# Performance work log

Measured on AMD Instinct MI355X. Metric: run time of the kernel, lower is better.

Reference implementation:

```python
import jax, jax.numpy as jnp
import numpy as np

# MoE config (matches init_kwargs): dim=512, num_experts=16, top_k=2, ffn mult=4
DIM = 512
NUM_EXPERTS = 16
TOP_K = 2
HIDDEN = 4 * DIM  # FeedForward inner dim
TOKENS = 2048
LN_EPS = 1e-5


def setup_inputs() -> dict:
    key = jax.random.key(0)
    ks = jax.random.split(key, 4)
    scaled = lambda k, shape, fan_in: (
        jax.random.normal(k, shape, dtype=jnp.float32) / np.sqrt(fan_in)
    )
    return {
        "x": jax.random.normal(ks[0], (TOKENS, DIM), dtype=jnp.float32),
        # gate: Linear(dim, num_experts, bias=False)
        "Wg": scaled(ks[1], (DIM, NUM_EXPERTS), DIM),
        # per-expert FFN params stacked on leading expert axis
        "W1": scaled(ks[2], (NUM_EXPERTS, DIM, HIDDEN), DIM),
        "b1": jnp.zeros((NUM_EXPERTS, HIDDEN), jnp.float32),
        "ln_g": jnp.ones((NUM_EXPERTS, HIDDEN), jnp.float32),
        "ln_b": jnp.zeros((NUM_EXPERTS, HIDDEN), jnp.float32),
        "W2": scaled(ks[3], (NUM_EXPERTS, HIDDEN, DIM), HIDDEN),
        "b2": jnp.zeros((NUM_EXPERTS, DIM), jnp.float32),
    }


def reference(x, Wg, W1, b1, ln_g, ln_b, W2, b2):
    # ---- routing ----
    gate_logits = x @ Wg                                   # [T, E]
    w, sel = jax.lax.top_k(gate_logits, TOP_K)             # [T, k]
    # softmax over the selected-experts axis, computed in fp32 (matches dtype=torch.float)
    w = jax.nn.softmax(w.astype(jnp.float32), axis=-1).astype(x.dtype)
    n_exp = Wg.shape[1]
    # combine[t, e] = sum_k w[t, k] * 1[sel[t, k] == e]
    combine = jnp.sum(
        w[..., None] * jax.nn.one_hot(sel, n_exp, dtype=x.dtype), axis=1
    )                                                      # [T, E]

    # ---- all experts (dense, jit-friendly dispatch) ----
    # FeedForward: Linear -> SiLU -> LayerNorm -> (Dropout=identity at eval) -> Linear
    h = jnp.einsum("td,edh->eth", x, W1) + b1[:, None, :]  # [E, T, H]
    h = jax.nn.silu(h)
    mu = jnp.mean(h, axis=-1, keepdims=True)
    var = jnp.mean(jnp.square(h - mu), axis=-1, keepdims=True)
    h = (h - mu) * jax.lax.rsqrt(var + LN_EPS)
    h = h * ln_g[:, None, :] + ln_b[:, None, :]
    y = jnp.einsum("eth,ehd->etd", h, W2) + b2[:, None, :]  # [E, T, D]

    # ---- weighted combine (scatter-add equivalent) ----
    return jnp.einsum("etd,te->td", y, combine)             # [T, D]
```

## Files before the change

### kernel.cpp

```cpp
#include <hip/hip_runtime.h>
#include <hip/hip_bf16.h>

#define TOKENS 2048
#define DIM 512
#define NEXP 16
#define HID 2048
#define CAP 320
#define NTPE (CAP / 64)
#define MTILES (NEXP * NTPE)
#define NROWS (NEXP * CAP)

typedef unsigned short ushort_t;
typedef __attribute__((ext_vector_type(8))) __bf16 bf16x8;
typedef __attribute__((ext_vector_type(4))) float f32x4;

#define OFF_CNT 0
#define OFF_LTOK 1024
#define OFF_LW 21504
#define OFF_S1 41984
#define OFF_S2 62464
#define OFF_XBF 82944
#define OFF_H 2180096
#define OFF_W1T 23151616
#define OFF_W2T 56706048

__device__ __forceinline__ ushort_t f2b(float f) {
  __bf16 b = (__bf16)f;
  return __builtin_bit_cast(unsigned short, b);
}
__device__ __forceinline__ float b2f(ushort_t u) {
  return __builtin_bit_cast(float, (unsigned)u << 16);
}

__global__ __launch_bounds__(256) void wconv_k(
    const float* __restrict__ W1, const float* __restrict__ W2,
    ushort_t* __restrict__ W1t, ushort_t* __restrict__ W2t,
    int* __restrict__ counts) {
  if (blockIdx.x == 0 && blockIdx.y == 0 && threadIdx.x < NEXP)
    counts[threadIdx.x] = 0;
  int bx = blockIdx.x;
  const float* src;
  ushort_t* dst;
  int K, N;
  if (bx < 256) { src = W1; dst = W1t; K = DIM; N = HID; }
  else { src = W2; dst = W2t; K = HID; N = DIM; bx -= 256; }
  int nnb = N >> 6;
  int bn = bx % nnb, bk = bx / nnb;
  int e = blockIdx.y;
  int t = threadIdx.x;
  int w = t >> 6, l = t & 63;
  int n = bn * 64 + l;
  int k_base = bk * 64;
  int kt0 = k_base >> 5;
  int kk = w * 8;

  const float* sp = src + ((size_t)e * K + k_base + kk) * N + n;
  float v[16];
#pragma unroll
  for (int j = 0; j < 8; j++) v[j] = sp[(size_t)j * N];
#pragma unroll
  for (int j = 0; j < 8; j++) v[8 + j] = sp[(size_t)(32 + j) * N];

  size_t tb = ((size_t)(e * (N >> 4) + (n >> 4)) * (K >> 5) + kt0) * 512 +
              (n & 15) * 32 + kk;
  union { ushort_t u[8]; uint4 q; } s0, s1;
#pragma unroll
  for (int j = 0; j < 8; j++) { s0.u[j] = f2b(v[j]); s1.u[j] = f2b(v[8 + j]); }
  *(uint4*)(dst + tb) = s0.q;
  *(uint4*)(dst + tb + 512) = s1.q;
}

__global__ __launch_bounds__(256) void router_k(
    const float* __restrict__ x, const float* __restrict__ Wg,
    ushort_t* __restrict__ xbf, int* __restrict__ counts,
    int* __restrict__ ltok, float* __restrict__ lw,
    float* __restrict__ s1, float* __restrict__ s2, float* __restrict__ out) {
  int t = threadIdx.x;
  {
    float4 z = {0.f, 0.f, 0.f, 0.f};
    float4* o4 = (float4*)out + blockIdx.x * 4096 + t;
#pragma unroll
    for (int i = 0; i < 16; i++) o4[i * 256] = z;
  }
  {
    int idx = blockIdx.x * 256 + t;
    if (idx < NROWS) { s1[idx] = 0.f; s2[idx] = 0.f; }
  }

  __shared__ float xs[4][512];
  __shared__ float lg[4][16];
  __shared__ int lcnt[NEXP];
  __shared__ int ltoks[NEXP][64];
  __shared__ float lws[NEXP][64];
  __shared__ int base_s[NEXP];

  if (t < NEXP) lcnt[t] = 0;
  __syncthreads();

  int lane = t & 63, w = t >> 6;
  int dq = lane >> 2, e4 = lane & 3;
  const float* wgp = Wg + dq * NEXP + e4 * 4;

  for (int it = 0; it < 8; it++) {
    int tok = blockIdx.x * 32 + w * 8 + it;
    const float* xr = x + (size_t)tok * DIM + lane * 8;
    float4 xa = *(const float4*)xr;
    float4 xb = *(const float4*)(xr + 4);
    union { ushort_t u[8]; uint4 v; } pk;
    pk.u[0] = f2b(xa.x); pk.u[1] = f2b(xa.y); pk.u[2] = f2b(xa.z); pk.u[3] = f2b(xa.w);
    pk.u[4] = f2b(xb.x); pk.u[5] = f2b(xb.y); pk.u[6] = f2b(xb.z); pk.u[7] = f2b(xb.w);
    *(uint4*)(xbf + (size_t)tok * DIM + lane * 8) = pk.v;
    *(float4*)&xs[w][lane * 8] = xa;
    *(float4*)&xs[w][lane * 8 + 4] = xb;

    float4 a = {0.f, 0.f, 0.f, 0.f};
#pragma unroll
    for (int kk = 0; kk < 32; kk++) {
      float xv = xs[w][kk * 16 + dq];
      float4 g = *(const float4*)(wgp + kk * 16 * NEXP);
      a.x += xv * g.x; a.y += xv * g.y; a.z += xv * g.z; a.w += xv * g.w;
    }
#pragma unroll
    for (int off = 32; off >= 4; off >>= 1) {
      a.x += __shfl_down(a.x, off);
      a.y += __shfl_down(a.y, off);
      a.z += __shfl_down(a.z, off);
      a.w += __shfl_down(a.w, off);
    }
    if (lane < 4) *(float4*)&lg[w][lane * 4] = a;
    if (lane == 0) {
      int i0 = 0;
      float v0 = lg[w][0];
#pragma unroll
      for (int e = 1; e < NEXP; e++)
        if (lg[w][e] > v0) { v0 = lg[w][e]; i0 = e; }
      int i1 = -1;
      float v1 = -3.4e38f;
#pragma unroll
      for (int e = 0; e < NEXP; e++)
        if (e != i0 && lg[w][e] > v1) { v1 = lg[w][e]; i1 = e; }
      float ex = __expf(v1 - v0);
      float w0 = 1.f / (1.f + ex);
      int p0 = atomicAdd(&lcnt[i0], 1);
      ltoks[i0][p0] = tok;
      lws[i0][p0] = w0;
      int p1 = atomicAdd(&lcnt[i1], 1);
      ltoks[i1][p1] = tok;
      lws[i1][p1] = ex / (1.f + ex);
    }
  }
  __syncthreads();
  if (t < NEXP) base_s[t] = atomicAdd(&counts[t], lcnt[t]);
  __syncthreads();
  int e = t >> 4, i0 = t & 15;
  int n = lcnt[e], b = base_s[e];
  for (int i = i0; i < n; i += 16) {
    int slot = b + i;
    if (slot < CAP) {
      ltok[e * CAP + slot] = ltoks[e][i];
      lw[e * CAP + slot] = lws[e][i];
    }
  }
}

__global__ __launch_bounds__(256) void ffn1_k(
    const ushort_t* __restrict__ W1t, const float* __restrict__ b1,
    const int* __restrict__ counts, const int* __restrict__ ltok,
    const ushort_t* __restrict__ xbf, ushort_t* __restrict__ hbuf,
    float* __restrict__ s1, float* __restrict__ s2) {
  int e = blockIdx.x / NTPE, mt = blockIdx.x % NTPE;
  int cnt = counts[e];
  if (cnt - mt * 64 <= 0) return;
  int row0 = e * CAP + mt * 64;
  int h0 = blockIdx.y * 256;

  __shared__ __align__(16) ushort_t As[2][64 * 40];

  int t = threadIdx.x;
  int lane = t & 63, wave = t >> 6;
  int quad = lane >> 4, l16 = lane & 15;

  int sr = t >> 2, sp = t & 3;
  int stok = ltok[row0 + sr];
  bool sok = (unsigned)stok < TOKENS;
  const ushort_t* sx = xbf + (size_t)(sok ? stok : 0) * DIM + sp * 8;

  int ncol = h0 + wave * 64 + l16;
  const ushort_t* bb = W1t +
      ((size_t)(e * 128 + (h0 >> 4) + wave * 4) * 16) * 512 + l16 * 32 + quad * 8;

  f32x4 acc[4][4];
#pragma unroll
  for (int a = 0; a < 4; a++)
#pragma unroll
    for (int b = 0; b < 4; b++) acc[a][b] = {0.f, 0.f, 0.f, 0.f};

  uint4 avB = {0u, 0u, 0u, 0u};
  {
    uint4 avA = {0u, 0u, 0u, 0u};
    if (sok) {
      avA = *(const uint4*)(sx);
      avB = *(const uint4*)(sx + 32);
    }
    *(uint4*)(&As[0][sr * 40 + sp * 8]) = avA;
  }
  bf16x8 bc[4];
#pragma unroll
  for (int nb = 0; nb < 4; nb++)
    bc[nb] = *(const bf16x8*)(bb + nb * 8192);

#pragma unroll
  for (int ks = 0; ks < 16; ks++) {
    __syncthreads();
    bf16x8 bn[4];
    if (ks < 15) {
#pragma unroll
      for (int nb = 0; nb < 4; nb++)
        bn[nb] = *(const bf16x8*)(bb + nb * 8192 + (ks + 1) * 512);
    }
    uint4 avN = {0u, 0u, 0u, 0u};
    if (ks < 14 && sok) avN = *(const uint4*)(sx + (ks + 2) * 32);

    bf16x8 af[4];
#pragma unroll
    for (int mb = 0; mb < 4; mb++)
      af[mb] = *(const bf16x8*)(&As[ks & 1][(mb * 16 + l16) * 40 + quad * 8]);
#pragma unroll
    for (int mb = 0; mb < 4; mb++)
#pragma unroll
      for (int nb = 0; nb < 4; nb++)
        acc[mb][nb] = __builtin_amdgcn_mfma_f32_16x16x32_bf16(af[mb], bc[nb], acc[mb][nb], 0, 0, 0);

    if (ks < 15) {
      *(uint4*)(&As[(ks + 1) & 1][sr * 40 + sp * 8]) = avB;
      avB = avN;
#pragma unroll
      for (int nb = 0; nb < 4; nb++) bc[nb] = bn[nb];
    }
  }

  float bia[4];
#pragma unroll
  for (int nb = 0; nb < 4; nb++) bia[nb] = b1[e * HID + ncol + nb * 16];
#pragma unroll
  for (int mb = 0; mb < 4; mb++) {
#pragma unroll
    for (int i = 0; i < 4; i++) {
      int m = mb * 16 + quad * 4 + i;
      size_t rowg = (size_t)(row0 + m);
      float ps = 0.f, qs = 0.f;
#pragma unroll
      for (int nb = 0; nb < 4; nb++) {
        float v = acc[mb][nb][i] + bia[nb];
        v = v / (1.f + __expf(-v));
        hbuf[rowg * HID + ncol + nb * 16] = f2b(v);
        ps += v;
        qs += v * v;
      }
      ps += __shfl_down(ps, 8); qs += __shfl_down(qs, 8);
      ps += __shfl_down(ps, 4); qs += __shfl_down(qs, 4);
      ps += __shfl_down(ps, 2); qs += __shfl_down(qs, 2);
      ps += __shfl_down(ps, 1); qs += __shfl_down(qs, 1);
      if (l16 == 0) {
        atomicAdd(&s1[rowg], ps);
        atomicAdd(&s2[rowg], qs);
      }
    }
  }
}

__global__ __launch_bounds__(256) void ffn2_k(
    const ushort_t* __restrict__ W2t, const float* __restrict__ b2,
    const float* __restrict__ lng, const float* __restrict__ lnb,
    const int* __restrict__ counts, const int* __restrict__ ltok,
    const float* __restrict__ lw, const ushort_t* __restrict__ hbuf,
    const float* __restrict__ s1, const float* __restrict__ s2,
    float* __restrict__ out) {
  int e = blockIdx.x / NTPE, mt = blockIdx.x % NTPE;
  int cnt = counts[e];
  int valid = cnt - mt * 64;
  if (valid <= 0) return;
  valid = valid > 64 ? 64 : valid;
  int row0 = e * CAP + mt * 64;
  int n0 = blockIdx.y * 256;
  int kbeg = blockIdx.z * (HID / 2);

  __shared__ __align__(16) ushort_t As[2][64 * 40];
  __shared__ float Gs[1024];
  __shared__ float Cs[1024];

  int t = threadIdx.x;
  int lane = t & 63, wave = t >> 6;
  int quad = lane >> 4, l16 = lane & 15;

  *(float4*)&Gs[t * 4] = *(const float4*)(lng + (size_t)e * HID + kbeg + t * 4);
  *(float4*)&Cs[t * 4] = *(const float4*)(lnb + (size_t)e * HID + kbeg + t * 4);

  int sr = t >> 2, sp = t & 3;
  size_t srow = (size_t)(row0 + sr);
  const ushort_t* hr = hbuf + srow * HID + kbeg + sp * 8;
  float smu = s1[srow] * (1.f / HID);
  float var = s2[srow] * (1.f / HID) - smu * smu;
  float srs = rsqrtf(var + 1e-5f);

  int ncol = n0 + wave * 64 + l16;
  const ushort_t* bb = W2t +
      ((size_t)(e * 32 + (n0 >> 4) + wave * 4) * 64 + blockIdx.z * 32) * 512 +
      l16 * 32 + quad * 8;

  f32x4 acc[4][4];
#pragma unroll
  for (int a = 0; a < 4; a++)
#pragma unroll
    for (int b = 0; b < 4; b++) acc[a][b] = {0.f, 0.f, 0.f, 0.f};

  uint4 hvA = *(const uint4*)(hr);
  uint4 hvB = *(const uint4*)(hr + 32);
  __syncthreads();

  {
    union { uint4 v; ushort_t u[8]; } hv;
    hv.v = hvA;
    int sb = sp * 8;
    union { ushort_t u[8]; uint4 v; } pk;
#pragma unroll
    for (int j = 0; j < 8; j++) {
      float f = (b2f(hv.u[j]) - smu) * srs;
      pk.u[j] = f2b(f * Gs[sb + j] + Cs[sb + j]);
    }
    *(uint4*)(&As[0][sr * 40 + sp * 8]) = pk.v;
  }
  bf16x8 bc[4];
#pragma unroll
  for (int nb = 0; nb < 4; nb++)
    bc[nb] = *(const bf16x8*)(bb + nb * 32768);

#pragma unroll 8
  for (int ks = 0; ks < 32; ks++) {
    __syncthreads();
    bf16x8 bn[4];
    if (ks < 31) {
#pragma unroll
      for (int nb = 0; nb < 4; nb++)
        bn[nb] = *(const bf16x8*)(bb + nb * 32768 + (ks + 1) * 512);
    }
    uint4 hvN = {0u, 0u, 0u, 0u};
    if (ks < 30) hvN = *(const uint4*)(hr + (ks + 2) * 32);

    bf16x8 af[4];
#pragma unroll
    for (int mb = 0; mb < 4; mb++)
      af[mb] = *(const bf16x8*)(&As[ks & 1][(mb * 16 + l16) * 40 + quad * 8]);
#pragma unroll
    for (int mb = 0; mb < 4; mb++)
#pragma unroll
      for (int nb = 0; nb < 4; nb++)
        acc[mb][nb] = __builtin_amdgcn_mfma_f32_16x16x32_bf16(af[mb], bc[nb], acc[mb][nb], 0, 0, 0);

    if (ks < 31) {
      union { uint4 v; ushort_t u[8]; } hv;
      hv.v = hvB;
      int sb = (ks + 1) * 32 + sp * 8;
      union { ushort_t u[8]; uint4 v; } pk;
#pragma unroll
      for (int j = 0; j < 8; j++) {
        float f = (b2f(hv.u[j]) - smu) * srs;
        pk.u[j] = f2b(f * Gs[sb + j] + Cs[sb + j]);
      }
      *(uint4*)(&As[(ks + 1) & 1][sr * 40 + sp * 8]) = pk.v;
      hvB = hvN;
#pragma unroll
      for (int nb = 0; nb < 4; nb++) bc[nb] = bn[nb];
    }
  }

  bool addb = (blockIdx.z == 0);
  float bia[4];
#pragma unroll
  for (int nb = 0; nb < 4; nb++)
    bia[nb] = addb ? b2[e * DIM + ncol + nb * 16] : 0.f;
#pragma unroll
  for (int mb = 0; mb < 4; mb++) {
#pragma unroll
    for (int i = 0; i < 4; i++) {
      int m = mb * 16 + quad * 4 + i;
      if (m < valid) {
        int tok = ltok[row0 + m];
        float w = lw[row0 + m];
#pragma unroll
        for (int nb = 0; nb < 4; nb++) {
          float v = acc[mb][nb][i] + bia[nb];
          atomicAdd(out + (size_t)tok * DIM + ncol + nb * 16, w * v);
        }
      }
    }
  }
}

extern "C" void kernel_launch(void* const* d_in, const int* in_sizes, int n_in,
                              void* d_out, int out_size, void* d_ws, size_t ws_size,
                              hipStream_t stream) {
  const float* x = (const float*)d_in[0];
  const float* Wg = (const float*)d_in[1];
  const float* W1 = (const float*)d_in[2];
  const float* b1 = (const float*)d_in[3];
  const float* lng = (const float*)d_in[4];
  const float* lnb = (const float*)d_in[5];
  const float* W2 = (const float*)d_in[6];
  const float* b2 = (const float*)d_in[7];
  float* out = (float*)d_out;

  char* ws = (char*)d_ws;
  int* counts = (int*)(ws + OFF_CNT);
  int* ltok = (int*)(ws + OFF_LTOK);
  float* lw = (float*)(ws + OFF_LW);
  float* s1 = (float*)(ws + OFF_S1);
  float* s2 = (float*)(ws + OFF_S2);
  ushort_t* xbf = (ushort_t*)(ws + OFF_XBF);
  ushort_t* hbuf = (ushort_t*)(ws + OFF_H);
  ushort_t* W1t = (ushort_t*)(ws + OFF_W1T);
  ushort_t* W2t = (ushort_t*)(ws + OFF_W2T);

  wconv_k<<<dim3(512, NEXP), 256, 0, stream>>>(W1, W2, W1t, W2t, counts);
  router_k<<<64, 256, 0, stream>>>(x, Wg, xbf, counts, ltok, lw, s1, s2, out);
  ffn1_k<<<dim3(MTILES, HID / 256), 256, 0, stream>>>(W1t, b1, counts, ltok, xbf, hbuf, s1, s2);
  ffn2_k<<<dim3(MTILES, DIM / 256, 2), 256, 0, stream>>>(W2t, b2, lng, lnb, counts, ltok,
                                                         lw, hbuf, s1, s2, out);
}
```

Before: 276.4 us.

## Store hidden activations in MFMA-tiled layout and load A fragments directly in ffn2

The first FFN kernel now writes the SiLU output into a 16x32 tiled layout that matches the MFMA operand fragment. The second kernel reads A fragments straight from global memory into registers, applying LayerNorm per lane with precomputed scale and shift. This removes the LDS staging buffer, the gamma/beta shared arrays and the per-iteration __syncthreads. The cost is that every wave now reloads and renormalizes the same A tiles redundantly, which adds global/L2 traffic and ALU work, and register pressure rises.

```diff
diff --git a/kernel.cpp b/kernel.cpp
--- a/kernel.cpp
+++ b/kernel.cpp
@@ -247,13 +247,15 @@
 #pragma unroll
     for (int i = 0; i < 4; i++) {
       int m = mb * 16 + quad * 4 + i;
-      size_t rowg = (size_t)(row0 + m);
+      int row = row0 + m;
       float ps = 0.f, qs = 0.f;
 #pragma unroll
       for (int nb = 0; nb < 4; nb++) {
         float v = acc[mb][nb][i] + bia[nb];
         v = v / (1.f + __expf(-v));
-        hbuf[rowg * HID + ncol + nb * 16] = f2b(v);
+        int col = ncol + nb * 16;
+        hbuf[((size_t)(row >> 4) * (HID / 32) + (col >> 5)) * 512 +
+             (row & 15) * 32 + (col & 31)] = f2b(v);
         ps += v;
         qs += v * v;
       }
@@ -262,8 +264,8 @@
       ps += __shfl_down(ps, 2); qs += __shfl_down(qs, 2);
       ps += __shfl_down(ps, 1); qs += __shfl_down(qs, 1);
       if (l16 == 0) {
-        atomicAdd(&s1[rowg], ps);
-        atomicAdd(&s2[rowg], qs);
+        atomicAdd(&s1[row], ps);
+        atomicAdd(&s2[row], qs);
       }
     }
   }
@@ -283,30 +285,32 @@
   valid = valid > 64 ? 64 : valid;
   int row0 = e * CAP + mt * 64;
   int n0 = blockIdx.y * 256;
+  int kt0 = blockIdx.z * 32;
   int kbeg = blockIdx.z * (HID / 2);
-
-  __shared__ __align__(16) ushort_t As[2][64 * 40];
-  __shared__ float Gs[1024];
-  __shared__ float Cs[1024];
 
   int t = threadIdx.x;
   int lane = t & 63, wave = t >> 6;
   int quad = lane >> 4, l16 = lane & 15;
 
-  *(float4*)&Gs[t * 4] = *(const float4*)(lng + (size_t)e * HID + kbeg + t * 4);
-  *(float4*)&Cs[t * 4] = *(const float4*)(lnb + (size_t)e * HID + kbeg + t * 4);
-
-  int sr = t >> 2, sp = t & 3;
-  size_t srow = (size_t)(row0 + sr);
-  const ushort_t* hr = hbuf + srow * HID + kbeg + sp * 8;
-  float smu = s1[srow] * (1.f / HID);
-  float var = s2[srow] * (1.f / HID) - smu * smu;
-  float srs = rsqrtf(var + 1e-5f);
+  float am[4], bm[4];
+#pragma unroll
+  for (int mb = 0; mb < 4; mb++) {
+    int r = row0 + mb * 16 + l16;
+    float mu = s1[r] * (1.f / HID);
+    float var = s2[r] * (1.f / HID) - mu * mu;
+    float srs = rsqrtf(var + 1e-5f);
+    am[mb] = srs;
+    bm[mb] = -mu * srs;
+  }
 
   int ncol = n0 + wave * 64 + l16;
   const ushort_t* bb = W2t +
-      ((size_t)(e * 32 + (n0 >> 4) + wave * 4) * 64 + blockIdx.z * 32) * 512 +
+      ((size_t)(e * 32 + (n0 >> 4) + wave * 4) * 64 + kt0) * 512 +
       l16 * 32 + quad * 8;
+  const ushort_t* ab = hbuf +
+      ((size_t)(row0 >> 4) * (HID / 32) + kt0) * 512 + l16 * 32 + quad * 8;
+  const float* gp = lng + (size_t)e * HID + kbeg + quad * 8;
+  const float* cp = lnb + (size_t)e * HID + kbeg + quad * 8;
 
   f32x4 acc[4][4];
 #pragma unroll
@@ -314,63 +318,62 @@
 #pragma unroll
     for (int b = 0; b < 4; b++) acc[a][b] = {0.f, 0.f, 0.f, 0.f};
 
-  uint4 hvA = *(const uint4*)(hr);
-  uint4 hvB = *(const uint4*)(hr + 32);
-  __syncthreads();
-
-  {
-    union { uint4 v; ushort_t u[8]; } hv;
-    hv.v = hvA;
-    int sb = sp * 8;
-    union { ushort_t u[8]; uint4 v; } pk;
-#pragma unroll
-    for (int j = 0; j < 8; j++) {
-      float f = (b2f(hv.u[j]) - smu) * srs;
-      pk.u[j] = f2b(f * Gs[sb + j] + Cs[sb + j]);
-    }
-    *(uint4*)(&As[0][sr * 40 + sp * 8]) = pk.v;
-  }
-  bf16x8 bc[4];
+  uint4 a_c[4], b_c[4];
+  float4 g0c, g1c, c0c, c1c;
+#pragma unroll
+  for (int mb = 0; mb < 4; mb++)
+    a_c[mb] = *(const uint4*)(ab + (size_t)mb * 32 * (HID / 32) * 512 / 2 * 0 + (size_t)mb * (HID / 32) * 512);
 #pragma unroll
   for (int nb = 0; nb < 4; nb++)
-    bc[nb] = *(const bf16x8*)(bb + nb * 32768);
-
-#pragma unroll 8
+    b_c[nb] = *(const uint4*)(bb + (size_t)nb * 16 * 2048 / 2 * 0 + (size_t)nb * 32768);
+  g0c = *(const float4*)gp; g1c = *(const float4*)(gp + 4);
+  c0c = *(const float4*)cp; c1c = *(const float4*)(cp + 4);
+
   for (int ks = 0; ks < 32; ks++) {
-    __syncthreads();
-    bf16x8 bn[4];
+    uint4 a_n[4], b_n[4];
+    float4 g0n, g1n, c0n, c1n;
     if (ks < 31) {
 #pragma unroll
+      for (int mb = 0; mb < 4; mb++)
+        a_n[mb] = *(const uint4*)(ab + (size_t)mb * (HID / 32) * 512 + (ks + 1) * 512);
+#pragma unroll
       for (int nb = 0; nb < 4; nb++)
-        bn[nb] = *(const bf16x8*)(bb + nb * 32768 + (ks + 1) * 512);
-    }
-    uint4 hvN = {0u, 0u, 0u, 0u};
-    if (ks < 30) hvN = *(const uint4*)(hr + (ks + 2) * 32);
-
+        b_n[nb] = *(const uint4*)(bb + (size_t)nb * 32768 + (ks + 1) * 512);
+      g0n = *(const float4*)(gp + (ks + 1) * 32);
+      g1n = *(const float4*)(gp + (ks + 1) * 32 + 4);
+      c0n = *(const float4*)(cp + (ks + 1) * 32);
+      c1n = *(const float4*)(cp + (ks + 1) * 32 + 4);
+    }
+
+    float g[8] = {g0c.x, g0c.y, g0c.z, g0c.w, g1c.x, g1c.y, g1c.z, g1c.w};
+    float be[8] = {c0c.x, c0c.y, c0c.z, c0c.w, c1c.x, c1c.y, c1c.z, c1c.w};
     bf16x8 af[4];
 #pragma unroll
+    for (int mb = 0; mb < 4; mb++) {
+      union { uint4 v; ushort_t u[8]; } hv;
+      hv.v = a_c[mb];
+      union { ushort_t u[8]; bf16x8 f; } o;
+#pragma unroll
+      for (int j = 0; j < 8; j++) {
+        float f = b2f(hv.u[j]);
+        float tv = f * am[mb] + bm[mb];
+        o.u[j] = f2b(tv * g[j] + be[j]);
+      }
+      af[mb] = o.f;
+    }
+#pragma unroll
     for (int mb = 0; mb < 4; mb++)
-      af[mb] = *(const bf16x8*)(&As[ks & 1][(mb * 16 + l16) * 40 + quad * 8]);
-#pragma unroll
-    for (int mb = 0; mb < 4; mb++)
 #pragma unroll
       for (int nb = 0; nb < 4; nb++)
-        acc[mb][nb] = __builtin_amdgcn_mfma_f32_16x16x32_bf16(af[mb], bc[nb], acc[mb][nb], 0, 0, 0);
+        acc[mb][nb] = __builtin_amdgcn_mfma_f32_16x16x32_bf16(
+            af[mb], __builtin_bit_cast(bf16x8, b_c[nb]), acc[mb][nb], 0, 0, 0);
 
     if (ks < 31) {
-      union { uint4 v; ushort_t u[8]; } hv;
-      hv.v = hvB;
-      int sb = (ks + 1) * 32 + sp * 8;
-      union { ushort_t u[8]; uint4 v; } pk;
-#pragma unroll
-      for (int j = 0; j < 8; j++) {
-        float f = (b2f(hv.u[j]) - smu) * srs;
-        pk.u[j] = f2b(f * Gs[sb + j] + Cs[sb + j]);
-      }
-      *(uint4*)(&As[(ks + 1) & 1][sr * 40 + sp * 8]) = pk.v;
-      hvB = hvN;
-#pragma unroll
-      for (int nb = 0; nb < 4; nb++) bc[nb] = bn[nb];
+#pragma unroll
+      for (int mb = 0; mb < 4; mb++) a_c[mb] = a_n[mb];
+#pragma unroll
+      for (int nb = 0; nb < 4; nb++) b_c[nb] = b_n[nb];
+      g0c = g0n; g1c = g1n; c0c = c0n; c1c = c1n;
     }
   }
 
```

New measurement: 478.0 us. 72.9% more time.

## Fuse weight conversion into router and FFN1 kernels to overlap stages

Applied to the files above, without the earlier changes.

Splits the weight conversion kernel. W1 conversion now runs as extra blocks inside the router kernel, and W2 conversion as extra blocks inside the FFN1 kernel. The counts reset moves to a hipMemsetAsync. The goal is to overlap the memory-bound weight transpose/convert with routing and the first GEMM, and to drop one launch boundary. It adds a memset launch, and the W2 conversion blocks now compete for CUs with FFN1 work.

```diff
diff --git a/kernel.cpp b/kernel.cpp
--- a/kernel.cpp
+++ b/kernel.cpp
@@ -32,58 +32,46 @@
   return __builtin_bit_cast(float, (unsigned)u << 16);
 }
 
-__global__ __launch_bounds__(256) void wconv_k(
-    const float* __restrict__ W1, const float* __restrict__ W2,
-    ushort_t* __restrict__ W1t, ushort_t* __restrict__ W2t,
-    int* __restrict__ counts) {
-  if (blockIdx.x == 0 && blockIdx.y == 0 && threadIdx.x < NEXP)
-    counts[threadIdx.x] = 0;
-  int bx = blockIdx.x;
-  const float* src;
-  ushort_t* dst;
-  int K, N;
-  if (bx < 256) { src = W1; dst = W1t; K = DIM; N = HID; }
-  else { src = W2; dst = W2t; K = HID; N = DIM; bx -= 256; }
-  int nnb = N >> 6;
-  int bn = bx % nnb, bk = bx / nnb;
-  int e = blockIdx.y;
+__global__ __launch_bounds__(256) void pre_k(
+    const float* __restrict__ x, const float* __restrict__ Wg,
+    const float* __restrict__ W1, ushort_t* __restrict__ xbf,
+    int* __restrict__ counts, int* __restrict__ ltok, float* __restrict__ lw,
+    float* __restrict__ s1, float* __restrict__ s2, float* __restrict__ out,
+    ushort_t* __restrict__ W1t) {
+  int bid = blockIdx.x;
   int t = threadIdx.x;
-  int w = t >> 6, l = t & 63;
-  int n = bn * 64 + l;
-  int k_base = bk * 64;
-  int kt0 = k_base >> 5;
-  int kk = w * 8;
-
-  const float* sp = src + ((size_t)e * K + k_base + kk) * N + n;
-  float v[16];
-#pragma unroll
-  for (int j = 0; j < 8; j++) v[j] = sp[(size_t)j * N];
-#pragma unroll
-  for (int j = 0; j < 8; j++) v[8 + j] = sp[(size_t)(32 + j) * N];
-
-  size_t tb = ((size_t)(e * (N >> 4) + (n >> 4)) * (K >> 5) + kt0) * 512 +
-              (n & 15) * 32 + kk;
-  union { ushort_t u[8]; uint4 q; } s0, s1;
-#pragma unroll
-  for (int j = 0; j < 8; j++) { s0.u[j] = f2b(v[j]); s1.u[j] = f2b(v[8 + j]); }
-  *(uint4*)(dst + tb) = s0.q;
-  *(uint4*)(dst + tb + 512) = s1.q;
-}
-
-__global__ __launch_bounds__(256) void router_k(
-    const float* __restrict__ x, const float* __restrict__ Wg,
-    ushort_t* __restrict__ xbf, int* __restrict__ counts,
-    int* __restrict__ ltok, float* __restrict__ lw,
-    float* __restrict__ s1, float* __restrict__ s2, float* __restrict__ out) {
-  int t = threadIdx.x;
+  if (bid >= 64) {
+    int idx = bid - 64;
+    int bx = idx & 255, e = idx >> 8;
+    int bn = bx & 31, bk = bx >> 5;
+    const int K = DIM, N = HID;
+    int w = t >> 6, l = t & 63;
+    int n = bn * 64 + l;
+    int k_base = bk * 64, kt0 = k_base >> 5, kk = w * 8;
+    const float* sp = W1 + ((size_t)e * K + k_base + kk) * N + n;
+    float v[16];
+#pragma unroll
+    for (int j = 0; j < 8; j++) v[j] = sp[(size_t)j * N];
+#pragma unroll
+    for (int j = 0; j < 8; j++) v[8 + j] = sp[(size_t)(32 + j) * N];
+    size_t tb = ((size_t)(e * (N >> 4) + (n >> 4)) * (K >> 5) + kt0) * 512 +
+                (n & 15) * 32 + kk;
+    union { ushort_t u[8]; uint4 q; } s0, s1u;
+#pragma unroll
+    for (int j = 0; j < 8; j++) { s0.u[j] = f2b(v[j]); s1u.u[j] = f2b(v[8 + j]); }
+    *(uint4*)(W1t + tb) = s0.q;
+    *(uint4*)(W1t + tb + 512) = s1u.q;
+    return;
+  }
+
   {
     float4 z = {0.f, 0.f, 0.f, 0.f};
-    float4* o4 = (float4*)out + blockIdx.x * 4096 + t;
+    float4* o4 = (float4*)out + bid * 4096 + t;
 #pragma unroll
     for (int i = 0; i < 16; i++) o4[i * 256] = z;
   }
   {
-    int idx = blockIdx.x * 256 + t;
+    int idx = bid * 256 + t;
     if (idx < NROWS) { s1[idx] = 0.f; s2[idx] = 0.f; }
   }
 
@@ -102,7 +90,7 @@
   const float* wgp = Wg + dq * NEXP + e4 * 4;
 
   for (int it = 0; it < 8; it++) {
-    int tok = blockIdx.x * 32 + w * 8 + it;
+    int tok = bid * 32 + w * 8 + it;
     const float* xr = x + (size_t)tok * DIM + lane * 8;
     float4 xa = *(const float4*)xr;
     float4 xb = *(const float4*)(xr + 4);
@@ -163,20 +151,47 @@
   }
 }
 
-__global__ __launch_bounds__(256) void ffn1_k(
+__global__ __launch_bounds__(256) void mid_k(
     const ushort_t* __restrict__ W1t, const float* __restrict__ b1,
     const int* __restrict__ counts, const int* __restrict__ ltok,
     const ushort_t* __restrict__ xbf, ushort_t* __restrict__ hbuf,
-    float* __restrict__ s1, float* __restrict__ s2) {
-  int e = blockIdx.x / NTPE, mt = blockIdx.x % NTPE;
+    float* __restrict__ s1, float* __restrict__ s2,
+    const float* __restrict__ W2, ushort_t* __restrict__ W2t) {
+  int bid = blockIdx.x;
+  int t = threadIdx.x;
+  if (bid >= 640) {
+    int idx = bid - 640;
+    int bx = idx & 255, e = idx >> 8;
+    int bn = bx & 7, bk = bx >> 3;
+    const int K = HID, N = DIM;
+    int w = t >> 6, l = t & 63;
+    int n = bn * 64 + l;
+    int k_base = bk * 64, kt0 = k_base >> 5, kk = w * 8;
+    const float* sp = W2 + ((size_t)e * K + k_base + kk) * N + n;
+    float v[16];
+#pragma unroll
+    for (int j = 0; j < 8; j++) v[j] = sp[(size_t)j * N];
+#pragma unroll
+    for (int j = 0; j < 8; j++) v[8 + j] = sp[(size_t)(32 + j) * N];
+    size_t tb = ((size_t)(e * (N >> 4) + (n >> 4)) * (K >> 5) + kt0) * 512 +
+                (n & 15) * 32 + kk;
+    union { ushort_t u[8]; uint4 q; } s0, s1u;
+#pragma unroll
+    for (int j = 0; j < 8; j++) { s0.u[j] = f2b(v[j]); s1u.u[j] = f2b(v[8 + j]); }
+    *(uint4*)(W2t + tb) = s0.q;
+    *(uint4*)(W2t + tb + 512) = s1u.q;
+    return;
+  }
+
+  int xb = bid % 80;
+  int e = xb / NTPE, mt = xb % NTPE;
   int cnt = counts[e];
   if (cnt - mt * 64 <= 0) return;
   int row0 = e * CAP + mt * 64;
-  int h0 = blockIdx.y * 256;
+  int h0 = (bid / 80) * 256;
 
   __shared__ __align__(16) ushort_t As[2][64 * 40];
 
-  int t = threadIdx.x;
   int lane = t & 63, wave = t >> 6;
   int quad = lane >> 4, l16 = lane & 15;
 
@@ -421,9 +436,12 @@
   ushort_t* W1t = (ushort_t*)(ws + OFF_W1T);
   ushort_t* W2t = (ushort_t*)(ws + OFF_W2T);
 
-  wconv_k<<<dim3(512, NEXP), 256, 0, stream>>>(W1, W2, W1t, W2t, counts);
-  router_k<<<64, 256, 0, stream>>>(x, Wg, xbf, counts, ltok, lw, s1, s2, out);
-  ffn1_k<<<dim3(MTILES, HID / 256), 256, 0, stream>>>(W1t, b1, counts, ltok, xbf, hbuf, s1, s2);
-  ffn2_k<<<dim3(MTILES, DIM / 256, 2), 256, 0, stream>>>(W2t, b2, lng, lnb, counts, ltok,
-                                                         lw, hbuf, s1, s2, out);
-}
+  hipMemsetAsync(counts, 0, NEXP * sizeof(int), stream);
+  pre_k<<<64 + 4096, 256, 0, stream>>>(x, Wg, W1, xbf, counts, ltok, lw,
+                                       s1, s2, out, W1t);
+  mid_k<<<640 + 4096, 256, 0, stream>>>(W1t, b1, counts, ltok, xbf, hbuf,
+                                        s1, s2, W2, W2t);
+  ffn2_k<<<dim3(MTILES, DIM / 256, 2), 256, 0, stream>>>(W2t, b2, lng, lnb,
+                                                         counts, ltok, lw,
+                                                         hbuf, s1, s2, out);
+}
```

Result: faster. 250.0 us (-9.6%).
